# Kernel optimization log

Measured on AMD Instinct MI355X. Metric: run time of the kernel, lower is better.

The kernel has to match this reference:

```python
import jax, jax.numpy as jnp
import numpy as np

H_HEADS = 8
DIM_HEAD = 64


def setup_inputs() -> dict:
    key = jax.random.key(0)
    ks = jax.random.split(key, 5)
    b, c, Hs, Ws = 16, 32, 128, 128
    qd = H_HEADS * c              # 256 (heads*c = Linear in_features)
    inner = H_HEADS * DIM_HEAD    # 512
    s = 0.02                      # keep logits in a sane range
    return {
        "x": jax.random.normal(ks[0], (b, c, Hs, Ws), jnp.float32),
        "Wq": jax.random.normal(ks[1], (inner, qd), jnp.float32) * s,
        "Wkv": jax.random.normal(ks[2], (2 * inner, qd), jnp.float32) * s,
        "Wout": jax.random.normal(ks[3], (qd, inner), jnp.float32) * s,
        "bout": jax.random.normal(ks[4], (qd,), jnp.float32) * s,
    }


def _proj(arg, W, bias=None):
    # apply_operator_or_ffn for nn.Linear:
    # rearrange '(b h) n d -> b d (h n)', Linear over last dim, then 'b d n -> b n d'
    B, n, d = arg.shape
    bp = B // H_HEADS
    t = arg.reshape(bp, H_HEADS, n, d)
    t = jnp.transpose(t, (0, 3, 1, 2)).reshape(bp, d, H_HEADS * n)  # [b', d, h*n]
    y = t @ W.T
    if bias is not None:
        y = y + bias
    return jnp.transpose(y, (0, 2, 1))  # [b', out_features, d]


def _split_heads(t):
    # 'b (h d) n -> (b h) d n'
    bp, hd, n = t.shape
    return t.reshape(bp, H_HEADS, hd // H_HEADS, n).reshape(bp * H_HEADS, hd // H_HEADS, n)


def reference(x, Wq, Wkv, Wout, bout):
    b, c = x.shape[0], x.shape[1]
    spatial = x.shape[2:]
    N = int(np.prod(spatial))
    scale = DIM_HEAD ** -0.5
    xf = x.reshape(b, c, N)
    q = _proj(xf, Wq)              # [b/h, inner, N]
    kv = _proj(xf, Wkv)            # [b/h, 2*inner, N]
    inner = q.shape[1]
    k, v = kv[:, :inner], kv[:, inner:]
    qh, kh, vh = _split_heads(q), _split_heads(k), _split_heads(v)  # [b, DIM_HEAD, N]
    sim = jnp.einsum('bin,bjn->bij', qh, kh) * scale                 # [b, dh, dh]
    attn = jax.nn.softmax(sim, axis=-1)
    out = jnp.einsum('bnj,bjd->bnd', attn, vh)                       # [b, dh, N]
    out = _proj(out, Wout, bout)                                     # [b/h, h*c, N]
    return out.reshape(b, c, *spatial)
```

## Files before the change

### kernel.cpp

```cpp
#include <hip/hip_runtime.h>
#include <cstdint>
#include <cstddef>

using u16 = unsigned short;
using u32 = unsigned int;

typedef __attribute__((ext_vector_type(8))) short bf16x8;
typedef __attribute__((ext_vector_type(16))) float f32x16;

__device__ __forceinline__ u16 f2bf(float f) {
  union { float f; u32 i; } x; x.f = f;
  u32 r = (x.i + 0x7FFFu + ((x.i >> 16) & 1u)) >> 16;
  return (u16)r;
}
__device__ __forceinline__ bf16x8 ldbf16x8(const u16* p) {
  union { uint4 u; bf16x8 v; } t;
  t.u = *(const uint4*)p;
  return t.v;
}

constexpr int NP = 16384;


constexpr size_t OFF_C   = 0;
constexpr size_t OFF_T   = 131072;
constexpr size_t OFF_AT  = 393216;
constexpr size_t OFF_WE  = 458752;
constexpr size_t OFF_MT  = 720896;
constexpr size_t OFF_MA  = 851968;
constexpr size_t OFF_XB  = 917504;
constexpr size_t OFF_XBT = 5111808;
constexpr size_t OFF_CP1 = 9306112;
constexpr size_t NEED1   = (OFF_CP1 + 4194304) * 4;
constexpr size_t OFF_CP2 = 851968;
constexpr size_t NEED2   = (OFF_CP2 + 6291456) * 4;

__global__ __launch_bounds__(256)
void k0_cvt(const float* __restrict__ x, u16* __restrict__ XbF,
            u16* __restrict__ XbTF) {
  __shared__ u32 Fs[256 * 33];
  const int pc = blockIdx.x;
  const int g  = blockIdx.y;
  const int p0 = pc * 64;
  const float* __restrict__ Xg = x + (size_t)g * 256 * NP;
  u16* __restrict__ XbFg  = XbF  + (size_t)g * 256 * NP;
  u16* __restrict__ XbTFg = XbTF + (size_t)g * NP * 256;
  const int tid = threadIdx.x;
  const int f8i = tid & 7, rb = tid >> 3;
  const int sA = pc * 4 + (f8i >> 1);
  const int hA = f8i & 1;
  for (int pass = 0; pass < 8; ++pass) {
    const int row = rb + pass * 32;
    const size_t e0 = (size_t)row * NP + p0 + f8i * 8;
    float4 a = *(const float4*)(Xg + e0);
    float4 b = *(const float4*)(Xg + e0 + 4);
    const float v[8] = {a.x, a.y, a.z, a.w, b.x, b.y, b.z, b.w};
    uint4 s;
    s.x = (u32)f2bf(v[0]) | ((u32)f2bf(v[1]) << 16);
    s.y = (u32)f2bf(v[2]) | ((u32)f2bf(v[3]) << 16);
    s.z = (u32)f2bf(v[4]) | ((u32)f2bf(v[5]) << 16);
    s.w = (u32)f2bf(v[6]) | ((u32)f2bf(v[7]) << 16);
    const int panel = row >> 5, lc = row & 31;
    *(uint4*)(XbFg + (size_t)panel * 524288 + sA * 512 + hA * 256 + lc * 8) = s;
    u32* d = &Fs[row * 33 + f8i * 4];
    d[0] = s.x; d[1] = s.y; d[2] = s.z; d[3] = s.w;
  }
  __syncthreads();
  const int p = tid & 63, grp = tid >> 6;
  const int pp = p0 + p;
  const int panelT = pp >> 5, lcT = pp & 31;
  const u16* __restrict__ Fs16 = (const u16*)Fs;
  u16* dstT = XbTFg + (size_t)panelT * 8192 + lcT * 8;
  for (int c = 0; c < 4; ++c) {
    const int sT = grp * 4 + c;
    u32 w[8];
#pragma unroll
    for (int q = 0; q < 8; ++q) {
      const int f = grp * 64 + c * 16 + q * 2;
      u32 lo = Fs16[f * 66 + p];
      u32 hi = Fs16[(f + 1) * 66 + p];
      w[q] = lo | (hi << 16);
    }
    uint4 s0 = {w[0], w[1], w[2], w[3]};
    uint4 s1 = {w[4], w[5], w[6], w[7]};
    *(uint4*)(dstT + sT * 512)       = s0;
    *(uint4*)(dstT + sT * 512 + 256) = s1;
  }
}

__global__ __launch_bounds__(256)
void k1_mfma(const u16* __restrict__ XbF, float* __restrict__ Cpart) {
  const int tp = blockIdx.x;
  const int kc = blockIdx.y;
  const int g  = blockIdx.z;
  const int ti = tp >> 1, tj = tp & 1;
  const int tid = threadIdx.x;
  const int w = tid >> 6, half = (tid >> 5) & 1, lc = tid & 31;
  const int qi = w >> 1, qj = w & 1;
  const u16* __restrict__ Xg = XbF + (size_t)g * 256 * NP;
  const size_t koff = (size_t)kc * 16384 + half * 256 + lc * 8;
  const u16* A0 = Xg + (size_t)(ti * 4 + qi * 2 + 0) * 524288 + koff;
  const u16* A1 = Xg + (size_t)(ti * 4 + qi * 2 + 1) * 524288 + koff;
  const u16* B0 = Xg + (size_t)(tj * 4 + qj * 2 + 0) * 524288 + koff;
  const u16* B1 = Xg + (size_t)(tj * 4 + qj * 2 + 1) * 524288 + koff;
  f32x16 acc00, acc01, acc10, acc11;
#pragma unroll
  for (int i = 0; i < 16; ++i) {
    acc00[i] = 0.f; acc01[i] = 0.f; acc10[i] = 0.f; acc11[i] = 0.f;
  }
#pragma unroll 4
  for (int s = 0; s < 32; ++s) {
    bf16x8 a0 = ldbf16x8(A0 + s * 512);
    bf16x8 a1 = ldbf16x8(A1 + s * 512);
    bf16x8 b0 = ldbf16x8(B0 + s * 512);
    bf16x8 b1 = ldbf16x8(B1 + s * 512);
    acc00 = __builtin_amdgcn_mfma_f32_32x32x16_bf16(a0, b0, acc00, 0, 0, 0);
    acc01 = __builtin_amdgcn_mfma_f32_32x32x16_bf16(a0, b1, acc01, 0, 0, 0);
    acc10 = __builtin_amdgcn_mfma_f32_32x32x16_bf16(a1, b0, acc10, 0, 0, 0);
    acc11 = __builtin_amdgcn_mfma_f32_32x32x16_bf16(a1, b1, acc11, 0, 0, 0);
  }
  float* __restrict__ P = Cpart + (((size_t)g * 4 + tp) * 32 + kc) * 16384;
#pragma unroll
  for (int r = 0; r < 16; ++r) {
    const int rr = (r & 3) + 8 * (r >> 2) + 4 * half;
    const int row0 = qi * 64 + rr, col0 = qj * 64 + lc;
    P[(row0 +  0) * 128 + col0 +  0] = acc00[r];
    P[(row0 +  0) * 128 + col0 + 32] = acc01[r];
    P[(row0 + 32) * 128 + col0 +  0] = acc10[r];
    P[(row0 + 32) * 128 + col0 + 32] = acc11[r];
  }
}

__global__ __launch_bounds__(256)
void k1b_red(const float* __restrict__ Cpart, float* __restrict__ Cmat) {
  const int sl = blockIdx.x;
  const int tp = blockIdx.y;
  const int g  = blockIdx.z;
  const int ele = sl * 256 + threadIdx.x;
  const float* __restrict__ P =
      Cpart + (((size_t)g * 4 + tp) * 32) * 16384 + ele;
  float v = 0.f;
#pragma unroll
  for (int kc = 0; kc < 32; ++kc) v += P[(size_t)kc * 16384];
  const int ti = tp >> 1, tj = tp & 1;
  const int i = ele >> 7, j = ele & 127;
  Cmat[(size_t)g * 65536 + (size_t)(ti * 128 + i) * 256 + tj * 128 + j] = v;
}

__global__ __launch_bounds__(256)
void k1_gram(const float* __restrict__ x, float* __restrict__ Cpart) {
  __shared__ float As[32 * 132];
  __shared__ float Bs[32 * 132];
  const int kc = blockIdx.x, ty = blockIdx.y, g = blockIdx.z;
  const int i0 = (ty == 2) ? 128 : 0;
  const int j0 = (ty == 0) ? 0 : 128;
  const float* __restrict__ Xg = x + (size_t)g * 256 * NP;
  const int tid = threadIdx.x, lane = tid & 63, w = tid >> 6;
  const int wy = (w >> 1) * 64, wx = (w & 1) * 64;
  const int ly = (lane >> 3) * 8, lx = (lane & 7) * 8;
  float acc[8][8];
#pragma unroll
  for (int e = 0; e < 8; ++e)
#pragma unroll
    for (int f = 0; f < 8; ++f) acc[e][f] = 0.f;
  const int k8 = (tid & 3) * 8, rowb = tid >> 2, k0 = kc * 256;
  for (int s = 0; s < 8; ++s) {
    const int ks = k0 + s * 32;
#pragma unroll
    for (int pass = 0; pass < 2; ++pass) {
      const int row = rowb + pass * 64;
      const size_t ea = (size_t)(i0 + row) * NP + ks + k8;
      float4 a = *(const float4*)(Xg + ea);
      float4 b = *(const float4*)(Xg + ea + 4);
      As[(k8+0)*132+row]=a.x; As[(k8+1)*132+row]=a.y;
      As[(k8+2)*132+row]=a.z; As[(k8+3)*132+row]=a.w;
      As[(k8+4)*132+row]=b.x; As[(k8+5)*132+row]=b.y;
      As[(k8+6)*132+row]=b.z; As[(k8+7)*132+row]=b.w;
      const size_t eb = (size_t)(j0 + row) * NP + ks + k8;
      a = *(const float4*)(Xg + eb);
      b = *(const float4*)(Xg + eb + 4);
      Bs[(k8+0)*132+row]=a.x; Bs[(k8+1)*132+row]=a.y;
      Bs[(k8+2)*132+row]=a.z; Bs[(k8+3)*132+row]=a.w;
      Bs[(k8+4)*132+row]=b.x; Bs[(k8+5)*132+row]=b.y;
      Bs[(k8+6)*132+row]=b.z; Bs[(k8+7)*132+row]=b.w;
    }
    __syncthreads();
#pragma unroll 4
    for (int kk = 0; kk < 32; ++kk) {
      const float* ar = &As[kk * 132 + wy + ly];
      const float* br = &Bs[kk * 132 + wx + lx];
      float4 a0 = *(const float4*)(ar), a1 = *(const float4*)(ar + 4);
      float4 b0 = *(const float4*)(br), b1 = *(const float4*)(br + 4);
      const float av[8] = {a0.x,a0.y,a0.z,a0.w,a1.x,a1.y,a1.z,a1.w};
      const float bv[8] = {b0.x,b0.y,b0.z,b0.w,b1.x,b1.y,b1.z,b1.w};
#pragma unroll
      for (int e = 0; e < 8; ++e)
#pragma unroll
        for (int f = 0; f < 8; ++f) acc[e][f] += av[e] * bv[f];
    }
    __syncthreads();
  }
  float* __restrict__ P = Cpart + (((size_t)g * 3 + ty) * 64 + kc) * 16384;
#pragma unroll
  for (int e = 0; e < 8; ++e) {
    float* pr = P + (size_t)(wy + ly + e) * 128 + wx + lx;
    float4 s0 = {acc[e][0], acc[e][1], acc[e][2], acc[e][3]};
    float4 s1 = {acc[e][4], acc[e][5], acc[e][6], acc[e][7]};
    *(float4*)(pr)     = s0;
    *(float4*)(pr + 4) = s1;
  }
}

__global__ __launch_bounds__(256)
void k1b_reduce(const float* __restrict__ Cpart, float* __restrict__ Cmat) {
  const int sl = blockIdx.x, ty = blockIdx.y, g = blockIdx.z;
  const int ele = sl * 256 + threadIdx.x;
  const float* __restrict__ P =
      Cpart + (((size_t)g * 3 + ty) * 64) * 16384 + ele;
  float v = 0.f;
#pragma unroll 8
  for (int kc = 0; kc < 64; ++kc) v += P[(size_t)kc * 16384];
  const int i0 = (ty == 2) ? 128 : 0;
  const int j0 = (ty == 0) ? 0 : 128;
  const int i = ele >> 7, j = ele & 127;
  float* Cg = Cmat + (size_t)g * 65536;
  Cg[(size_t)(i0 + i) * 256 + (j0 + j)] = v;
  if (ty == 1) Cg[(size_t)(j0 + j) * 256 + (i0 + i)] = v;
}

__global__ __launch_bounds__(256)
void k1_gram_atomic(const float* __restrict__ x, float* __restrict__ Cmat) {
  __shared__ float As[32 * 132];
  __shared__ float Bs[32 * 132];
  const int kc = blockIdx.x, ty = blockIdx.y, g = blockIdx.z;
  const int i0 = (ty == 2) ? 128 : 0;
  const int j0 = (ty == 0) ? 0 : 128;
  const float* __restrict__ Xg = x + (size_t)g * 256 * NP;
  const int tid = threadIdx.x, lane = tid & 63, w = tid >> 6;
  const int wy = (w >> 1) * 64, wx = (w & 1) * 64;
  const int ly = (lane >> 3) * 8, lx = (lane & 7) * 8;
  float acc[8][8];
#pragma unroll
  for (int e = 0; e < 8; ++e)
#pragma unroll
    for (int f = 0; f < 8; ++f) acc[e][f] = 0.f;
  const int k8 = (tid & 3) * 8, rowb = tid >> 2, k0 = kc * 256;
  for (int s = 0; s < 8; ++s) {
    const int ks = k0 + s * 32;
#pragma unroll
    for (int pass = 0; pass < 2; ++pass) {
      const int row = rowb + pass * 64;
      const size_t ea = (size_t)(i0 + row) * NP + ks + k8;
      float4 a = *(const float4*)(Xg + ea);
      float4 b = *(const float4*)(Xg + ea + 4);
      As[(k8+0)*132+row]=a.x; As[(k8+1)*132+row]=a.y;
      As[(k8+2)*132+row]=a.z; As[(k8+3)*132+row]=a.w;
      As[(k8+4)*132+row]=b.x; As[(k8+5)*132+row]=b.y;
      As[(k8+6)*132+row]=b.z; As[(k8+7)*132+row]=b.w;
      const size_t eb = (size_t)(j0 + row) * NP + ks + k8;
      a = *(const float4*)(Xg + eb);
      b = *(const float4*)(Xg + eb + 4);
      Bs[(k8+0)*132+row]=a.x; Bs[(k8+1)*132+row]=a.y;
      Bs[(k8+2)*132+row]=a.z; Bs[(k8+3)*132+row]=a.w;
      Bs[(k8+4)*132+row]=b.x; Bs[(k8+5)*132+row]=b.y;
      Bs[(k8+6)*132+row]=b.z; Bs[(k8+7)*132+row]=b.w;
    }
    __syncthreads();
#pragma unroll 4
    for (int kk = 0; kk < 32; ++kk) {
      const float* ar = &As[kk * 132 + wy + ly];
      const float* br = &Bs[kk * 132 + wx + lx];
      float4 a0 = *(const float4*)(ar), a1 = *(const float4*)(ar + 4);
      float4 b0 = *(const float4*)(br), b1 = *(const float4*)(br + 4);
      const float av[8] = {a0.x,a0.y,a0.z,a0.w,a1.x,a1.y,a1.z,a1.w};
      const float bv[8] = {b0.x,b0.y,b0.z,b0.w,b1.x,b1.y,b1.z,b1.w};
#pragma unroll
      for (int e = 0; e < 8; ++e)
#pragma unroll
        for (int f = 0; f < 8; ++f) acc[e][f] += av[e] * bv[f];
    }
    __syncthreads();
  }
  float* Cg = Cmat + (size_t)g * 65536;
#pragma unroll
  for (int e = 0; e < 8; ++e)
#pragma unroll
    for (int f = 0; f < 8; ++f) {
      atomicAdd(&Cg[(i0+wy+ly+e)*256 + (j0+wx+lx+f)], acc[e][f]);
      if (ty == 1)
        atomicAdd(&Cg[(j0+wx+lx+f)*256 + (i0+wy+ly+e)], acc[e][f]);
    }
}

__global__ __launch_bounds__(256)
void kA_attn(const float* __restrict__ Wq, const float* __restrict__ Wkv,
             const float* __restrict__ Cmat, float* __restrict__ attn) {
  __shared__ float WqL[4 * 256];
  __shared__ float Ts[4 * 256];
  const int bh = blockIdx.x;
  const int ic = blockIdx.y;
  const int g = bh >> 3, hh = bh & 7;
  const int tid = threadIdx.x;
  const float* __restrict__ Cg = Cmat + (size_t)g * 65536;
  {
    const int r = tid >> 6, c4 = (tid & 63) * 4;
    *(float4*)(&WqL[r * 256 + c4]) =
        *(const float4*)(Wq + (size_t)(hh * 64 + ic * 4 + r) * 256 + c4);
  }
  __syncthreads();
  float acc[4] = {0.f, 0.f, 0.f, 0.f};
#pragma unroll 8
  for (int b = 0; b < 256; ++b) {
    const float cv = Cg[(size_t)b * 256 + tid];
#pragma unroll
    for (int r = 0; r < 4; ++r) acc[r] += WqL[r * 256 + b] * cv;
  }
#pragma unroll
  for (int r = 0; r < 4; ++r) Ts[r * 256 + tid] = acc[r];
  __syncthreads();
  const int r = tid >> 6, j = tid & 63;
  const float* __restrict__ Wk = Wkv + (size_t)(hh * 64 + j) * 256;
  float s = 0.f;
#pragma unroll 4
  for (int a4 = 0; a4 < 64; ++a4) {
    float4 w = *(const float4*)(Wk + a4 * 4);
    const float* t4 = &Ts[r * 256 + a4 * 4];
    s += t4[0] * w.x + t4[1] * w.y + t4[2] * w.z + t4[3] * w.w;
  }
  s *= 0.125f;
  float m = s;
#pragma unroll
  for (int off = 32; off; off >>= 1) m = fmaxf(m, __shfl_xor(m, off));
  const float e = __expf(s - m);
  float sum = e;
#pragma unroll
  for (int off = 32; off; off >>= 1) sum += __shfl_xor(sum, off);
  attn[((size_t)bh * 64 + ic * 4 + r) * 64 + j] = e / sum;
}

__global__ __launch_bounds__(256)
void kB_m(const float* __restrict__ Wout, const float* __restrict__ Wkv,
          const float* __restrict__ attn, float* __restrict__ Mp) {
  __shared__ float AtL[64 * 64];
  __shared__ float WoL[16 * 64];
  __shared__ float UL[16 * 64];
  const int bh = blockIdx.x;
  const int cc = blockIdx.y;
  const int g = bh >> 3, hh = bh & 7;
  const int tid = threadIdx.x;
  {
    const float* __restrict__ A = attn + (size_t)bh * 4096;
#pragma unroll
    for (int q = 0; q < 4; ++q)
      *(float4*)(&AtL[q * 1024 + tid * 4]) =
          *(const float4*)(A + q * 1024 + tid * 4);
  }
  {
    const int co_l = tid >> 4, i4 = (tid & 15) * 4;
    *(float4*)(&WoL[co_l * 64 + i4]) =
        *(const float4*)(Wout + (size_t)(cc * 16 + co_l) * 512 + hh * 64 + i4);
  }
  __syncthreads();
  const int j = tid & 63, cw = tid >> 6;
  float u4[4] = {0.f, 0.f, 0.f, 0.f};
#pragma unroll 4
  for (int i = 0; i < 64; ++i) {
    const float av = AtL[i * 64 + j];
#pragma unroll
    for (int u = 0; u < 4; ++u) u4[u] += WoL[(cw * 4 + u) * 64 + i] * av;
  }
  __syncthreads();
#pragma unroll
  for (int u = 0; u < 4; ++u) UL[(cw * 4 + u) * 64 + j] = u4[u];
  __syncthreads();
  float acc[16];
#pragma unroll
  for (int c = 0; c < 16; ++c) acc[c] = 0.f;
#pragma unroll 4
  for (int j2 = 0; j2 < 64; ++j2) {
    const float wv = Wkv[(size_t)(512 + hh * 64 + j2) * 256 + tid];
#pragma unroll
    for (int c = 0; c < 16; ++c) acc[c] += UL[c * 64 + j2] * wv;
  }
  float* __restrict__ P =
      Mp + (((size_t)g * 8 + hh) * 256 + cc * 16) * 256 + tid;
#pragma unroll
  for (int c = 0; c < 16; ++c) P[(size_t)c * 256] = acc[c];
}

__global__ __launch_bounds__(256)
void kC_red(const float* __restrict__ Mp, u16* __restrict__ MA) {
  const int panel = blockIdx.x >> 2;
  const int q     = blockIdx.x & 3;
  const int g     = blockIdx.y;
  const int tid = threadIdx.x;
  const float* __restrict__ Pg = Mp + (size_t)g * 8 * 65536;
  u16* __restrict__ Mg = MA + (size_t)g * 65536;
  const int item = tid + q * 256;
  const int lc = item & 31;
  const int co = panel * 32 + lc;
  const int b0 = (item >> 5) * 8;
  float v[8] = {0.f, 0.f, 0.f, 0.f, 0.f, 0.f, 0.f, 0.f};
#pragma unroll
  for (int hd = 0; hd < 8; ++hd) {
    const float* p = Pg + (size_t)hd * 65536 + (size_t)co * 256 + b0;
    float4 a = *(const float4*)(p);
    float4 b = *(const float4*)(p + 4);
    v[0] += a.x; v[1] += a.y; v[2] += a.z; v[3] += a.w;
    v[4] += b.x; v[5] += b.y; v[6] += b.z; v[7] += b.w;
  }
  uint4 sdat;
  sdat.x = (u32)f2bf(v[0]) | ((u32)f2bf(v[1]) << 16);
  sdat.y = (u32)f2bf(v[2]) | ((u32)f2bf(v[3]) << 16);
  sdat.z = (u32)f2bf(v[4]) | ((u32)f2bf(v[5]) << 16);
  sdat.w = (u32)f2bf(v[6]) | ((u32)f2bf(v[7]) << 16);
  *(uint4*)(Mg + (size_t)panel * 8192 + (size_t)item * 8) = sdat;
}

__global__ __launch_bounds__(256) void k2_T(const float* __restrict__ Wq,
                                            const float* __restrict__ Cmat,
                                            float* __restrict__ T) {
  const int bh = blockIdx.x;
  const int ic = blockIdx.y;
  const int g = bh >> 3, hh = bh & 7;
  const int tid = threadIdx.x;
  const float* __restrict__ Cg = Cmat + (size_t)g * 65536;
  const int r0 = hh * 64 + ic * 4;
  float acc[4] = {0.f, 0.f, 0.f, 0.f};
#pragma unroll 8
  for (int b = 0; b < 256; ++b) {
    const float cv = Cg[(size_t)b * 256 + tid];
#pragma unroll
    for (int ii = 0; ii < 4; ++ii)
      acc[ii] += Wq[(size_t)(r0 + ii) * 256 + b] * cv;
  }
#pragma unroll
  for (int ii = 0; ii < 4; ++ii)
    T[((size_t)bh * 64 + ic * 4 + ii) * 256 + tid] = acc[ii];
}

__global__ __launch_bounds__(256) void k3_sim(const float* __restrict__ Wkv,
                                              const float* __restrict__ T,
                                              float* __restrict__ simattn) {
  __shared__ float Ts[64 * 256];
  const int bh = blockIdx.x;
  const int jc = blockIdx.y;
  const int hh = bh & 7;
  const int tid = threadIdx.x;
  {
    const int f4i = tid & 63;
    const int rwb = tid >> 6;
    for (int pass = 0; pass < 16; ++pass) {
      const int row = rwb + pass * 4;
      float4 v = *(const float4*)(T + ((size_t)bh * 64 + row) * 256 + f4i * 4);
      const int a0 = f4i * 4;
      const float vv[4] = {v.x, v.y, v.z, v.w};
#pragma unroll
      for (int e = 0; e < 4; ++e) {
        const int a = a0 + e;
        Ts[row * 256 + (a & ~31) + ((a + row) & 31)] = vv[e];
      }
    }
  }
  __syncthreads();
  const int i  = tid & 63;
  const int jq = tid >> 6;
  const int jb = jc * 16 + jq * 4;
  float acc[4] = {0.f, 0.f, 0.f, 0.f};
#pragma unroll 4
  for (int a = 0; a < 256; ++a) {
    const float tv = Ts[i * 256 + (a & ~31) + ((a + i) & 31)];
#pragma unroll
    for (int jj = 0; jj < 4; ++jj)
      acc[jj] += Wkv[(size_t)(hh * 64 + jb + jj) * 256 + a] * tv;
  }
#pragma unroll
  for (int jj = 0; jj < 4; ++jj)
    simattn[((size_t)bh * 64 + i) * 64 + jb + jj] = acc[jj] * 0.125f;
}

__global__ __launch_bounds__(64) void k3b_softmax(float* __restrict__ simattn) {
  const int bh = blockIdx.x;
  const int i  = threadIdx.x;
  float* row = simattn + ((size_t)bh * 64 + i) * 64;
  float v[64];
  float m = -1e30f;
#pragma unroll
  for (int j = 0; j < 64; ++j) { v[j] = row[j]; m = fmaxf(m, v[j]); }
  float s = 0.f;
#pragma unroll
  for (int j = 0; j < 64; ++j) { v[j] = __expf(v[j] - m); s += v[j]; }
  const float inv = 1.0f / s;
#pragma unroll
  for (int j = 0; j < 64; ++j) row[j] = v[j] * inv;
}

__global__ __launch_bounds__(256) void k4_we(const float* __restrict__ Wout,
                                             const float* __restrict__ attn,
                                             float* __restrict__ WeT) {
  __shared__ float WL[256 * 64];
  const int jc = blockIdx.x;
  const int hh = blockIdx.y;
  const int g  = blockIdx.z;
  const int bh = g * 8 + hh;
  const int tid = threadIdx.x;
  {
    const int f4i = tid & 15;
    const int cb  = tid >> 4;
    for (int pass = 0; pass < 16; ++pass) {
      const int co = cb + pass * 16;
      float4 v = *(const float4*)(Wout + (size_t)co * 512 + hh * 64 + f4i * 4);
      const int a0 = f4i * 4;
      const float vv[4] = {v.x, v.y, v.z, v.w};
#pragma unroll
      for (int e = 0; e < 4; ++e)
        WL[co * 64 + ((a0 + e + co) & 63)] = vv[e];
    }
  }
  __syncthreads();
  const int jb = jc * 8;
  float acc[8] = {0.f, 0.f, 0.f, 0.f, 0.f, 0.f, 0.f, 0.f};
#pragma unroll 4
  for (int i = 0; i < 64; ++i) {
    const float wv = WL[tid * 64 + ((i + tid) & 63)];
#pragma unroll
    for (int je = 0; je < 8; ++je)
      acc[je] += attn[((size_t)bh * 64 + i) * 64 + jb + je] * wv;
  }
#pragma unroll
  for (int je = 0; je < 8; ++je)
    WeT[(size_t)g * 131072 + (size_t)(hh * 64 + jb + je) * 256 + tid] =
        acc[je];
}

__global__ __launch_bounds__(256)
void k5a_part(const float* __restrict__ Wkv, const float* __restrict__ WeT,
              float* __restrict__ Mp) {
  const int bc = blockIdx.x;
  const int oc = blockIdx.y;
  const int g  = blockIdx.z;
  const int tid = threadIdx.x;
  const int b0 = bc * 4;
  const float* __restrict__ Weg = WeT + (size_t)g * 131072;
  float acc[4] = {0.f, 0.f, 0.f, 0.f};
#pragma unroll 8
  for (int u = 0; u < 32; ++u) {
    const int o = oc * 32 + u;
    const float wv = Weg[(size_t)o * 256 + tid];
    const float* __restrict__ vr = Wkv + (size_t)(512 + o) * 256 + b0;
    acc[0] += vr[0] * wv;
    acc[1] += vr[1] * wv;
    acc[2] += vr[2] * wv;
    acc[3] += vr[3] * wv;
  }
#pragma unroll
  for (int be = 0; be < 4; ++be)
    Mp[(((size_t)g * 16 + oc) * 256 + b0 + be) * 256 + tid] = acc[be];
}

__global__ __launch_bounds__(256)
void k5b_red(const float* __restrict__ Mp, float* __restrict__ Mt,
             u16* __restrict__ MA) {
  const int b = blockIdx.x;
  const int g = blockIdx.y;
  const int tid = threadIdx.x;
  const float* __restrict__ P =
      Mp + ((size_t)g * 16 * 256 + b) * 256 + tid;
  float v = 0.f;
#pragma unroll
  for (int oc = 0; oc < 16; ++oc) v += P[(size_t)oc * 65536];
  Mt[(size_t)g * 65536 + (size_t)b * 256 + tid] = v;
  MA[(size_t)g * 65536 + (size_t)tid * 256 + b] = f2bf(v);
}

__global__ __launch_bounds__(256) void k5_serial(const float* __restrict__ Wkv,
                                                 const float* __restrict__ WeT,
                                                 float* __restrict__ Mt,
                                                 u16* __restrict__ MA) {
  const int bc = blockIdx.x;
  const int g  = blockIdx.y;
  const int tid = threadIdx.x;
  const int b0 = bc * 4;
  const float* __restrict__ Weg = WeT + (size_t)g * 131072;
  float acc[4] = {0.f, 0.f, 0.f, 0.f};
#pragma unroll 4
  for (int o = 0; o < 512; ++o) {
    const float wv = Weg[(size_t)o * 256 + tid];
    const float* __restrict__ vr = Wkv + (size_t)(512 + o) * 256 + b0;
    acc[0] += vr[0] * wv;
    acc[1] += vr[1] * wv;
    acc[2] += vr[2] * wv;
    acc[3] += vr[3] * wv;
  }
#pragma unroll
  for (int be = 0; be < 4; ++be) {
    Mt[(size_t)g * 65536 + (size_t)(b0 + be) * 256 + tid] = acc[be];
    MA[(size_t)g * 65536 + (size_t)tid * 256 + b0 + be] = f2bf(acc[be]);
  }
}

__global__ __launch_bounds__(256)
void k6_mfma(const u16* __restrict__ XbTF, const u16* __restrict__ MA,
             const float* __restrict__ bout, float* __restrict__ out) {
  const int pb = blockIdx.x;
  const int cb = blockIdx.y;
  const int g  = blockIdx.z;
  const int tid = threadIdx.x;
  const int w = tid >> 6, half = (tid >> 5) & 1, lc = tid & 31;
  const int p0  = pb * 128 + w * 32;
  const int co0 = cb * 128;
  const u16* __restrict__ Ap = XbTF + (size_t)g * NP * 256 +
                               (size_t)(pb * 4 + w) * 8192 + half * 256 +
                               lc * 8;
  const u16* __restrict__ Bp = MA + (size_t)g * 65536 +
                               (size_t)cb * 32768 + half * 256 + lc * 8;
  f32x16 acc[4];
#pragma unroll
  for (int t = 0; t < 4; ++t)
#pragma unroll
    for (int i = 0; i < 16; ++i) acc[t][i] = 0.f;
#pragma unroll 2
  for (int s = 0; s < 16; ++s) {
    bf16x8 a = ldbf16x8(Ap + s * 512);
#pragma unroll
    for (int t = 0; t < 4; ++t) {
      bf16x8 b = ldbf16x8(Bp + (size_t)t * 8192 + s * 512);
      acc[t] = __builtin_amdgcn_mfma_f32_32x32x16_bf16(a, b, acc[t], 0, 0, 0);
    }
  }
#pragma unroll
  for (int t = 0; t < 4; ++t) {
    const int co = co0 + t * 32 + lc;
    const float bo = bout[co];
    float* __restrict__ ocol =
        out + ((size_t)(g * 256 + co)) * NP + p0 + 4 * half;
#pragma unroll
    for (int rg = 0; rg < 4; ++rg) {
      float4 v = {acc[t][rg * 4 + 0] + bo, acc[t][rg * 4 + 1] + bo,
                  acc[t][rg * 4 + 2] + bo, acc[t][rg * 4 + 3] + bo};
      *(float4*)(ocol + rg * 8) = v;
    }
  }
}

__global__ __launch_bounds__(256)
void k6_apply(const float* __restrict__ x, const float* __restrict__ Mt,
              const float* __restrict__ bout, float* __restrict__ out) {
  __shared__ float As[32 * 132];
  __shared__ float Bs[32 * 132];
  const int pc = blockIdx.x;
  const int oy = blockIdx.y;
  const int g  = blockIdx.z;
  const int p0 = pc * 128;
  const int o0 = oy * 128;
  const float* __restrict__ Xg = x + (size_t)g * 256 * NP;
  const float* __restrict__ Mg = Mt + (size_t)g * 65536;
  const int tid  = threadIdx.x;
  const int lane = tid & 63;
  const int w    = tid >> 6;
  const int wy = (w >> 1) * 64;
  const int wx = (w & 1) * 64;
  const int ly = (lane >> 3) * 8;
  const int lx = (lane & 7) * 8;
  float acc[8][8];
#pragma unroll
  for (int e = 0; e < 8; ++e)
#pragma unroll
    for (int f = 0; f < 8; ++f) acc[e][f] = 0.f;
  const int c4 = (tid & 31) * 4;
  const int kb = tid >> 5;
  for (int s = 0; s < 8; ++s) {
#pragma unroll
    for (int r = 0; r < 4; ++r) {
      const int kk = kb + r * 8;
      const int f  = s * 32 + kk;
      *(float4*)&As[kk * 132 + c4] =
          *(const float4*)(Mg + (size_t)f * 256 + o0 + c4);
      *(float4*)&Bs[kk * 132 + c4] =
          *(const float4*)(Xg + (size_t)f * NP + p0 + c4);
    }
    __syncthreads();
#pragma unroll 4
    for (int kk = 0; kk < 32; ++kk) {
      const float* __restrict__ ar = &As[kk * 132 + wy + ly];
      const float* __restrict__ br = &Bs[kk * 132 + wx + lx];
      float4 a0 = *(const float4*)(ar);
      float4 a1 = *(const float4*)(ar + 4);
      float4 b0 = *(const float4*)(br);
      float4 b1 = *(const float4*)(br + 4);
      const float av[8] = {a0.x, a0.y, a0.z, a0.w, a1.x, a1.y, a1.z, a1.w};
      const float bv[8] = {b0.x, b0.y, b0.z, b0.w, b1.x, b1.y, b1.z, b1.w};
#pragma unroll
      for (int e = 0; e < 8; ++e)
#pragma unroll
        for (int f = 0; f < 8; ++f) acc[e][f] += av[e] * bv[f];
    }
    __syncthreads();
  }
#pragma unroll
  for (int e = 0; e < 8; ++e) {
    const int co = o0 + wy + ly + e;
    const float bo = bout[co];
    float* __restrict__ orow =
        out + ((size_t)(g * 256 + co)) * NP + p0 + wx + lx;
    float4 s0 = {acc[e][0] + bo, acc[e][1] + bo, acc[e][2] + bo,
                 acc[e][3] + bo};
    float4 s1 = {acc[e][4] + bo, acc[e][5] + bo, acc[e][6] + bo,
                 acc[e][7] + bo};
    *(float4*)(orow)     = s0;
    *(float4*)(orow + 4) = s1;
  }
}

extern "C" void kernel_launch(void* const* d_in, const int* in_sizes, int n_in,
                              void* d_out, int out_size, void* d_ws,
                              size_t ws_size, hipStream_t stream) {
  const float* x    = (const float*)d_in[0];
  const float* Wq   = (const float*)d_in[1];
  const float* Wkv  = (const float*)d_in[2];
  const float* Wout = (const float*)d_in[3];
  const float* bout = (const float*)d_in[4];
  float* out = (float*)d_out;
  float* ws  = (float*)d_ws;

  float* C    = ws + OFF_C;
  float* T    = ws + OFF_T;
  float* att  = ws + OFF_AT;
  float* WeT  = ws + OFF_WE;
  float* Mt   = ws + OFF_MT;
  u16*   MA   = (u16*)(ws + OFF_MA);
  u16*   Xb   = (u16*)(ws + OFF_XB);
  u16*   XbT  = (u16*)(ws + OFF_XBT);
  float* Cp1  = ws + OFF_CP1;
  float* Cp2  = ws + OFF_CP2;

  const bool mfma_path = (ws_size >= NEED1);
  const bool splitk    = (ws_size >= NEED2);

  if (mfma_path) {
    k0_cvt<<<dim3(256, 2), 256, 0, stream>>>(x, Xb, XbT);
    k1_mfma<<<dim3(4, 32, 2), 256, 0, stream>>>(Xb, Cp1);
    k1b_red<<<dim3(64, 4, 2), 256, 0, stream>>>(Cp1, C);
    kA_attn<<<dim3(16, 16), 256, 0, stream>>>(Wq, Wkv, C, att);
    kB_m<<<dim3(16, 16), 256, 0, stream>>>(Wout, Wkv, att, Cp1);
    kC_red<<<dim3(32, 2), 256, 0, stream>>>(Cp1, MA);
    k6_mfma<<<dim3(128, 2, 2), 256, 0, stream>>>(XbT, MA, bout, out);
    return;
  }

  if (splitk) {
    k1_gram<<<dim3(64, 3, 2), 256, 0, stream>>>(x, Cp2);
    k1b_reduce<<<dim3(64, 3, 2), 256, 0, stream>>>(Cp2, C);
  } else {
    hipMemsetAsync(C, 0, 131072 * sizeof(float), stream);
    k1_gram_atomic<<<dim3(64, 3, 2), 256, 0, stream>>>(x, C);
  }
  k2_T<<<dim3(16, 16), 256, 0, stream>>>(Wq, C, T);
  k3_sim<<<dim3(16, 4), 256, 0, stream>>>(Wkv, T, att);
  k3b_softmax<<<dim3(16), 64, 0, stream>>>(att);
  k4_we<<<dim3(8, 8, 2), 256, 0, stream>>>(Wout, att, WeT);
  if (splitk) {
    k5a_part<<<dim3(64, 16, 2), 256, 0, stream>>>(Wkv, WeT, Cp2);
    k5b_red<<<dim3(256, 2), 256, 0, stream>>>(Cp2, Mt, MA);
  } else {
    k5_serial<<<dim3(64, 2), 256, 0, stream>>>(Wkv, WeT, Mt, MA);
  }
  k6_apply<<<dim3(128, 2, 2), 256, 0, stream>>>(x, Mt, bout, out);
}
```

Baseline: 159.3 us.

## Fuse all pipeline stages into one cooperative persistent kernel with grid syncs

Merges the seven separate kernels (bf16 convert, Gram MFMA, split-K reduce, attention, M build, M reduce, output MFMA) into a single cooperative kernel of 512 blocks, with grid.sync() between stages. This removes per-kernel launch overhead and inter-kernel gaps in a pipeline made of many small stages. In exchange, many stages use only 64–256 of the 512 blocks and each grid barrier has its own cost. The NEED1 workspace threshold is bumped slightly, and the old multi-kernel path stays as a fallback if the cooperative launch fails.

Measured after the change: 491.6 us. +208.7%, slower.

```diff
diff --git a/kernel.cpp b/kernel.cpp
--- a/kernel.cpp
+++ b/kernel.cpp
@@ -1,6 +1,9 @@
 #include <hip/hip_runtime.h>
+#include <hip/hip_cooperative_groups.h>
 #include <cstdint>
 #include <cstddef>
+
+namespace cg = cooperative_groups;
 
 using u16 = unsigned short;
 using u32 = unsigned int;
@@ -31,9 +34,283 @@
 constexpr size_t OFF_XB  = 917504;
 constexpr size_t OFF_XBT = 5111808;
 constexpr size_t OFF_CP1 = 9306112;
-constexpr size_t NEED1   = (OFF_CP1 + 4194304) * 4;
+constexpr size_t NEED1   = (OFF_CP1 + 4194304 + 4) * 4;
 constexpr size_t OFF_CP2 = 851968;
 constexpr size_t NEED2   = (OFF_CP2 + 6291456) * 4;
+
+__global__ __launch_bounds__(256, 2)
+void fused_all(const float* __restrict__ x, const float* __restrict__ Wq,
+               const float* __restrict__ Wkv, const float* __restrict__ Wout,
+               const float* __restrict__ bout, float* __restrict__ out,
+               u16* __restrict__ XbF, u16* __restrict__ XbTF,
+               float* __restrict__ Cmat, float* __restrict__ attn,
+               u16* __restrict__ MA, float* __restrict__ Cpart) {
+  __shared__ __align__(16) u32 shm[256 * 33];
+  cg::grid_group grid = cg::this_grid();
+  const int bid = blockIdx.x;
+  const int tid = threadIdx.x;
+
+  {
+    const int pc = bid >> 1, g = bid & 1;
+    const int p0 = pc * 64;
+    const float* __restrict__ Xg = x + (size_t)g * 256 * NP;
+    u16* __restrict__ XbFg  = XbF  + (size_t)g * 256 * NP;
+    u16* __restrict__ XbTFg = XbTF + (size_t)g * NP * 256;
+    const int f8i = tid & 7, rb = tid >> 3;
+    const int sA = pc * 4 + (f8i >> 1);
+    const int hA = f8i & 1;
+    u32* Fs = shm;
+    for (int pass = 0; pass < 8; ++pass) {
+      const int row = rb + pass * 32;
+      const size_t e0 = (size_t)row * NP + p0 + f8i * 8;
+      float4 a = *(const float4*)(Xg + e0);
+      float4 b = *(const float4*)(Xg + e0 + 4);
+      const float v[8] = {a.x, a.y, a.z, a.w, b.x, b.y, b.z, b.w};
+      uint4 s;
+      s.x = (u32)f2bf(v[0]) | ((u32)f2bf(v[1]) << 16);
+      s.y = (u32)f2bf(v[2]) | ((u32)f2bf(v[3]) << 16);
+      s.z = (u32)f2bf(v[4]) | ((u32)f2bf(v[5]) << 16);
+      s.w = (u32)f2bf(v[6]) | ((u32)f2bf(v[7]) << 16);
+      const int panel = row >> 5, lc = row & 31;
+      *(uint4*)(XbFg + (size_t)panel * 524288 + sA * 512 + hA * 256 + lc * 8) =
+          s;
+      u32* d = &Fs[row * 33 + f8i * 4];
+      d[0] = s.x; d[1] = s.y; d[2] = s.z; d[3] = s.w;
+    }
+    __syncthreads();
+    const int p = tid & 63, grp = tid >> 6;
+    const int pp = p0 + p;
+    const int panelT = pp >> 5, lcT = pp & 31;
+    const u16* __restrict__ Fs16 = (const u16*)Fs;
+    u16* dstT = XbTFg + (size_t)panelT * 8192 + lcT * 8;
+    for (int c = 0; c < 4; ++c) {
+      const int sT = grp * 4 + c;
+      u32 w[8];
+#pragma unroll
+      for (int q = 0; q < 8; ++q) {
+        const int f = grp * 64 + c * 16 + q * 2;
+        u32 lo = Fs16[f * 66 + p];
+        u32 hi = Fs16[(f + 1) * 66 + p];
+        w[q] = lo | (hi << 16);
+      }
+      uint4 s0 = {w[0], w[1], w[2], w[3]};
+      uint4 s1 = {w[4], w[5], w[6], w[7]};
+      *(uint4*)(dstT + sT * 512)       = s0;
+      *(uint4*)(dstT + sT * 512 + 256) = s1;
+    }
+  }
+  grid.sync();
+
+  if (bid < 256) {
+    const int tp = bid >> 6, kc = (bid >> 1) & 31, g = bid & 1;
+    const int ti = tp >> 1, tj = tp & 1;
+    const int w = tid >> 6, half = (tid >> 5) & 1, lc = tid & 31;
+    const int qi = w >> 1, qj = w & 1;
+    const u16* __restrict__ Xg = XbF + (size_t)g * 256 * NP;
+    const size_t koff = (size_t)kc * 16384 + half * 256 + lc * 8;
+    const u16* A0 = Xg + (size_t)(ti * 4 + qi * 2 + 0) * 524288 + koff;
+    const u16* A1 = Xg + (size_t)(ti * 4 + qi * 2 + 1) * 524288 + koff;
+    const u16* B0 = Xg + (size_t)(tj * 4 + qj * 2 + 0) * 524288 + koff;
+    const u16* B1 = Xg + (size_t)(tj * 4 + qj * 2 + 1) * 524288 + koff;
+    f32x16 acc00, acc01, acc10, acc11;
+#pragma unroll
+    for (int i = 0; i < 16; ++i) {
+      acc00[i] = 0.f; acc01[i] = 0.f; acc10[i] = 0.f; acc11[i] = 0.f;
+    }
+#pragma unroll 4
+    for (int s = 0; s < 32; ++s) {
+      bf16x8 a0 = ldbf16x8(A0 + s * 512);
+      bf16x8 a1 = ldbf16x8(A1 + s * 512);
+      bf16x8 b0 = ldbf16x8(B0 + s * 512);
+      bf16x8 b1 = ldbf16x8(B1 + s * 512);
+      acc00 = __builtin_amdgcn_mfma_f32_32x32x16_bf16(a0, b0, acc00, 0, 0, 0);
+      acc01 = __builtin_amdgcn_mfma_f32_32x32x16_bf16(a0, b1, acc01, 0, 0, 0);
+      acc10 = __builtin_amdgcn_mfma_f32_32x32x16_bf16(a1, b0, acc10, 0, 0, 0);
+      acc11 = __builtin_amdgcn_mfma_f32_32x32x16_bf16(a1, b1, acc11, 0, 0, 0);
+    }
+    float* __restrict__ P = Cpart + (((size_t)g * 4 + tp) * 32 + kc) * 16384;
+#pragma unroll
+    for (int r = 0; r < 16; ++r) {
+      const int rr = (r & 3) + 8 * (r >> 2) + 4 * half;
+      const int row0 = qi * 64 + rr, col0 = qj * 64 + lc;
+      P[(row0 +  0) * 128 + col0 +  0] = acc00[r];
+      P[(row0 +  0) * 128 + col0 + 32] = acc01[r];
+      P[(row0 + 32) * 128 + col0 +  0] = acc10[r];
+      P[(row0 + 32) * 128 + col0 + 32] = acc11[r];
+    }
+  }
+  grid.sync();
+
+  {
+    const int sl = bid >> 3, tp = (bid >> 1) & 3, g = bid & 1;
+    const int ele = sl * 256 + tid;
+    const float* __restrict__ P =
+        Cpart + (((size_t)g * 4 + tp) * 32) * 16384 + ele;
+    float v = 0.f;
+#pragma unroll
+    for (int kc = 0; kc < 32; ++kc) v += P[(size_t)kc * 16384];
+    const int ti = tp >> 1, tj = tp & 1;
+    const int i = ele >> 7, j = ele & 127;
+    Cmat[(size_t)g * 65536 + (size_t)(ti * 128 + i) * 256 + tj * 128 + j] = v;
+  }
+  grid.sync();
+
+  if (bid < 256) {
+    float* WqL = (float*)shm;
+    float* Ts  = (float*)shm + 1024;
+    const int bh = bid >> 4, ic = bid & 15;
+    const int g = bh >> 3, hh = bh & 7;
+    const float* __restrict__ Cg = Cmat + (size_t)g * 65536;
+    {
+      const int r = tid >> 6, c4 = (tid & 63) * 4;
+      *(float4*)(&WqL[r * 256 + c4]) =
+          *(const float4*)(Wq + (size_t)(hh * 64 + ic * 4 + r) * 256 + c4);
+    }
+    __syncthreads();
+    float acc[4] = {0.f, 0.f, 0.f, 0.f};
+#pragma unroll 8
+    for (int b = 0; b < 256; ++b) {
+      const float cv = Cg[(size_t)b * 256 + tid];
+#pragma unroll
+      for (int r = 0; r < 4; ++r) acc[r] += WqL[r * 256 + b] * cv;
+    }
+#pragma unroll
+    for (int r = 0; r < 4; ++r) Ts[r * 256 + tid] = acc[r];
+    __syncthreads();
+    const int r = tid >> 6, j = tid & 63;
+    const float* __restrict__ Wk = Wkv + (size_t)(hh * 64 + j) * 256;
+    float s = 0.f;
+#pragma unroll 4
+    for (int a4 = 0; a4 < 64; ++a4) {
+      float4 w = *(const float4*)(Wk + a4 * 4);
+      const float* t4 = &Ts[r * 256 + a4 * 4];
+      s += t4[0] * w.x + t4[1] * w.y + t4[2] * w.z + t4[3] * w.w;
+    }
+    s *= 0.125f;
+    float m = s;
+#pragma unroll
+    for (int off = 32; off; off >>= 1) m = fmaxf(m, __shfl_xor(m, off));
+    const float e = __expf(s - m);
+    float sum = e;
+#pragma unroll
+    for (int off = 32; off; off >>= 1) sum += __shfl_xor(sum, off);
+    attn[((size_t)bh * 64 + ic * 4 + r) * 64 + j] = e / sum;
+  }
+  grid.sync();
+
+  if (bid < 256) {
+    float* AtL = (float*)shm;
+    float* WoL = (float*)shm + 4096;
+    float* UL  = (float*)shm + 5120;
+    const int bh = bid >> 4, cc = bid & 15;
+    const int g = bh >> 3, hh = bh & 7;
+    {
+      const float* __restrict__ A = attn + (size_t)bh * 4096;
+#pragma unroll
+      for (int q = 0; q < 4; ++q)
+        *(float4*)(&AtL[q * 1024 + tid * 4]) =
+            *(const float4*)(A + q * 1024 + tid * 4);
+    }
+    {
+      const int co_l = tid >> 4, i4 = (tid & 15) * 4;
+      *(float4*)(&WoL[co_l * 64 + i4]) = *(const float4*)(
+          Wout + (size_t)(cc * 16 + co_l) * 512 + hh * 64 + i4);
+    }
+    __syncthreads();
+    const int j = tid & 63, cw = tid >> 6;
+    float u4[4] = {0.f, 0.f, 0.f, 0.f};
+#pragma unroll 4
+    for (int i = 0; i < 64; ++i) {
+      const float av = AtL[i * 64 + j];
+#pragma unroll
+      for (int u = 0; u < 4; ++u) u4[u] += WoL[(cw * 4 + u) * 64 + i] * av;
+    }
+    __syncthreads();
+#pragma unroll
+    for (int u = 0; u < 4; ++u) UL[(cw * 4 + u) * 64 + j] = u4[u];
+    __syncthreads();
+    float acc[16];
+#pragma unroll
+    for (int c = 0; c < 16; ++c) acc[c] = 0.f;
+#pragma unroll 4
+    for (int j2 = 0; j2 < 64; ++j2) {
+      const float wv = Wkv[(size_t)(512 + hh * 64 + j2) * 256 + tid];
+#pragma unroll
+      for (int c = 0; c < 16; ++c) acc[c] += UL[c * 64 + j2] * wv;
+    }
+    float* __restrict__ P =
+        Cpart + (((size_t)g * 8 + hh) * 256 + cc * 16) * 256 + tid;
+#pragma unroll
+    for (int c = 0; c < 16; ++c) P[(size_t)c * 256] = acc[c];
+  }
+  grid.sync();
+
+  if (bid < 64) {
+    const int xx = bid >> 1, g = bid & 1;
+    const int panel = xx >> 2, q = xx & 3;
+    const float* __restrict__ Pg = Cpart + (size_t)g * 8 * 65536;
+    u16* __restrict__ Mg = MA + (size_t)g * 65536;
+    const int item = tid + q * 256;
+    const int lc = item & 31;
+    const int co = panel * 32 + lc;
+    const int b0 = (item >> 5) * 8;
+    float v[8] = {0.f, 0.f, 0.f, 0.f, 0.f, 0.f, 0.f, 0.f};
+#pragma unroll
+    for (int hd = 0; hd < 8; ++hd) {
+      const float* p = Pg + (size_t)hd * 65536 + (size_t)co * 256 + b0;
+      float4 a = *(const float4*)(p);
+      float4 b = *(const float4*)(p + 4);
+      v[0] += a.x; v[1] += a.y; v[2] += a.z; v[3] += a.w;
+      v[4] += b.x; v[5] += b.y; v[6] += b.z; v[7] += b.w;
+    }
+    uint4 sdat;
+    sdat.x = (u32)f2bf(v[0]) | ((u32)f2bf(v[1]) << 16);
+    sdat.y = (u32)f2bf(v[2]) | ((u32)f2bf(v[3]) << 16);
+    sdat.z = (u32)f2bf(v[4]) | ((u32)f2bf(v[5]) << 16);
+    sdat.w = (u32)f2bf(v[6]) | ((u32)f2bf(v[7]) << 16);
+    *(uint4*)(Mg + (size_t)panel * 8192 + (size_t)item * 8) = sdat;
+  }
+  grid.sync();
+
+  {
+    const int pb = bid >> 2, cb = (bid >> 1) & 1, g = bid & 1;
+    const int w = tid >> 6, half = (tid >> 5) & 1, lc = tid & 31;
+    const int p0  = pb * 128 + w * 32;
+    const int co0 = cb * 128;
+    const u16* __restrict__ Ap = XbTF + (size_t)g * NP * 256 +
+                                 (size_t)(pb * 4 + w) * 8192 + half * 256 +
+                                 lc * 8;
+    const u16* __restrict__ Bp =
+        MA + (size_t)g * 65536 + (size_t)cb * 32768 + half * 256 + lc * 8;
+    f32x16 acc[4];
+#pragma unroll
+    for (int t = 0; t < 4; ++t)
+#pragma unroll
+      for (int i = 0; i < 16; ++i) acc[t][i] = 0.f;
+#pragma unroll 2
+    for (int s = 0; s < 16; ++s) {
+      bf16x8 a = ldbf16x8(Ap + s * 512);
+#pragma unroll
+      for (int t = 0; t < 4; ++t) {
+        bf16x8 b = ldbf16x8(Bp + (size_t)t * 8192 + s * 512);
+        acc[t] = __builtin_amdgcn_mfma_f32_32x32x16_bf16(a, b, acc[t], 0, 0, 0);
+      }
+    }
+#pragma unroll
+    for (int t = 0; t < 4; ++t) {
+      const int co = co0 + t * 32 + lc;
+      const float bo = bout[co];
+      float* __restrict__ ocol =
+          out + ((size_t)(g * 256 + co)) * NP + p0 + 4 * half;
+#pragma unroll
+      for (int rg = 0; rg < 4; ++rg) {
+        float4 v = {acc[t][rg * 4 + 0] + bo, acc[t][rg * 4 + 1] + bo,
+                    acc[t][rg * 4 + 2] + bo, acc[t][rg * 4 + 3] + bo};
+        *(float4*)(ocol + rg * 8) = v;
+      }
+    }
+  }
+}
 
 __global__ __launch_bounds__(256)
 void k0_cvt(const float* __restrict__ x, u16* __restrict__ XbF,
@@ -148,6 +425,175 @@
 }
 
 __global__ __launch_bounds__(256)
+void kA_attn(const float* __restrict__ Wq, const float* __restrict__ Wkv,
+             const float* __restrict__ Cmat, float* __restrict__ attn) {
+  __shared__ float WqL[4 * 256];
+  __shared__ float Ts[4 * 256];
+  const int bh = blockIdx.x;
+  const int ic = blockIdx.y;
+  const int g = bh >> 3, hh = bh & 7;
+  const int tid = threadIdx.x;
+  const float* __restrict__ Cg = Cmat + (size_t)g * 65536;
+  {
+    const int r = tid >> 6, c4 = (tid & 63) * 4;
+    *(float4*)(&WqL[r * 256 + c4]) =
+        *(const float4*)(Wq + (size_t)(hh * 64 + ic * 4 + r) * 256 + c4);
+  }
+  __syncthreads();
+  float acc[4] = {0.f, 0.f, 0.f, 0.f};
+#pragma unroll 8
+  for (int b = 0; b < 256; ++b) {
+    const float cv = Cg[(size_t)b * 256 + tid];
+#pragma unroll
+    for (int r = 0; r < 4; ++r) acc[r] += WqL[r * 256 + b] * cv;
+  }
+#pragma unroll
+  for (int r = 0; r < 4; ++r) Ts[r * 256 + tid] = acc[r];
+  __syncthreads();
+  const int r = tid >> 6, j = tid & 63;
+  const float* __restrict__ Wk = Wkv + (size_t)(hh * 64 + j) * 256;
+  float s = 0.f;
+#pragma unroll 4
+  for (int a4 = 0; a4 < 64; ++a4) {
+    float4 w = *(const float4*)(Wk + a4 * 4);
+    const float* t4 = &Ts[r * 256 + a4 * 4];
+    s += t4[0] * w.x + t4[1] * w.y + t4[2] * w.z + t4[3] * w.w;
+  }
+  s *= 0.125f;
+  float m = s;
+#pragma unroll
+  for (int off = 32; off; off >>= 1) m = fmaxf(m, __shfl_xor(m, off));
+  const float e = __expf(s - m);
+  float sum = e;
+#pragma unroll
+  for (int off = 32; off; off >>= 1) sum += __shfl_xor(sum, off);
+  attn[((size_t)bh * 64 + ic * 4 + r) * 64 + j] = e / sum;
+}
+
+__global__ __launch_bounds__(256)
+void kB_m(const float* __restrict__ Wout, const float* __restrict__ Wkv,
+          const float* __restrict__ attn, float* __restrict__ Mp) {
+  __shared__ float AtL[64 * 64];
+  __shared__ float WoL[16 * 64];
+  __shared__ float UL[16 * 64];
+  const int bh = blockIdx.x;
+  const int cc = blockIdx.y;
+  const int g = bh >> 3, hh = bh & 7;
+  const int tid = threadIdx.x;
+  {
+    const float* __restrict__ A = attn + (size_t)bh * 4096;
+#pragma unroll
+    for (int q = 0; q < 4; ++q)
+      *(float4*)(&AtL[q * 1024 + tid * 4]) =
+          *(const float4*)(A + q * 1024 + tid * 4);
+  }
+  {
+    const int co_l = tid >> 4, i4 = (tid & 15) * 4;
+    *(float4*)(&WoL[co_l * 64 + i4]) =
+        *(const float4*)(Wout + (size_t)(cc * 16 + co_l) * 512 + hh * 64 + i4);
+  }
+  __syncthreads();
+  const int j = tid & 63, cw = tid >> 6;
+  float u4[4] = {0.f, 0.f, 0.f, 0.f};
+#pragma unroll 4
+  for (int i = 0; i < 64; ++i) {
+    const float av = AtL[i * 64 + j];
+#pragma unroll
+    for (int u = 0; u < 4; ++u) u4[u] += WoL[(cw * 4 + u) * 64 + i] * av;
+  }
+  __syncthreads();
+#pragma unroll
+  for (int u = 0; u < 4; ++u) UL[(cw * 4 + u) * 64 + j] = u4[u];
+  __syncthreads();
+  float acc[16];
+#pragma unroll
+  for (int c = 0; c < 16; ++c) acc[c] = 0.f;
+#pragma unroll 4
+  for (int j2 = 0; j2 < 64; ++j2) {
+    const float wv = Wkv[(size_t)(512 + hh * 64 + j2) * 256 + tid];
+#pragma unroll
+    for (int c = 0; c < 16; ++c) acc[c] += UL[c * 64 + j2] * wv;
+  }
+  float* __restrict__ P =
+      Mp + (((size_t)g * 8 + hh) * 256 + cc * 16) * 256 + tid;
+#pragma unroll
+  for (int c = 0; c < 16; ++c) P[(size_t)c * 256] = acc[c];
+}
+
+__global__ __launch_bounds__(256)
+void kC_red(const float* __restrict__ Mp, u16* __restrict__ MA) {
+  const int panel = blockIdx.x >> 2;
+  const int q     = blockIdx.x & 3;
+  const int g     = blockIdx.y;
+  const int tid = threadIdx.x;
+  const float* __restrict__ Pg = Mp + (size_t)g * 8 * 65536;
+  u16* __restrict__ Mg = MA + (size_t)g * 65536;
+  const int item = tid + q * 256;
+  const int lc = item & 31;
+  const int co = panel * 32 + lc;
+  const int b0 = (item >> 5) * 8;
+  float v[8] = {0.f, 0.f, 0.f, 0.f, 0.f, 0.f, 0.f, 0.f};
+#pragma unroll
+  for (int hd = 0; hd < 8; ++hd) {
+    const float* p = Pg + (size_t)hd * 65536 + (size_t)co * 256 + b0;
+    float4 a = *(const float4*)(p);
+    float4 b = *(const float4*)(p + 4);
+    v[0] += a.x; v[1] += a.y; v[2] += a.z; v[3] += a.w;
+    v[4] += b.x; v[5] += b.y; v[6] += b.z; v[7] += b.w;
+  }
+  uint4 sdat;
+  sdat.x = (u32)f2bf(v[0]) | ((u32)f2bf(v[1]) << 16);
+  sdat.y = (u32)f2bf(v[2]) | ((u32)f2bf(v[3]) << 16);
+  sdat.z = (u32)f2bf(v[4]) | ((u32)f2bf(v[5]) << 16);
+  sdat.w = (u32)f2bf(v[6]) | ((u32)f2bf(v[7]) << 16);
+  *(uint4*)(Mg + (size_t)panel * 8192 + (size_t)item * 8) = sdat;
+}
+
+__global__ __launch_bounds__(256)
+void k6_mfma(const u16* __restrict__ XbTF, const u16* __restrict__ MA,
+             const float* __restrict__ bout, float* __restrict__ out) {
+  const int pb = blockIdx.x;
+  const int cb = blockIdx.y;
+  const int g  = blockIdx.z;
+  const int tid = threadIdx.x;
+  const int w = tid >> 6, half = (tid >> 5) & 1, lc = tid & 31;
+  const int p0  = pb * 128 + w * 32;
+  const int co0 = cb * 128;
+  const u16* __restrict__ Ap = XbTF + (size_t)g * NP * 256 +
+                               (size_t)(pb * 4 + w) * 8192 + half * 256 +
+                               lc * 8;
+  const u16* __restrict__ Bp = MA + (size_t)g * 65536 +
+                               (size_t)cb * 32768 + half * 256 + lc * 8;
+  f32x16 acc[4];
+#pragma unroll
+  for (int t = 0; t < 4; ++t)
+#pragma unroll
+    for (int i = 0; i < 16; ++i) acc[t][i] = 0.f;
+#pragma unroll 2
+  for (int s = 0; s < 16; ++s) {
+    bf16x8 a = ldbf16x8(Ap + s * 512);
+#pragma unroll
+    for (int t = 0; t < 4; ++t) {
+      bf16x8 b = ldbf16x8(Bp + (size_t)t * 8192 + s * 512);
+      acc[t] = __builtin_amdgcn_mfma_f32_32x32x16_bf16(a, b, acc[t], 0, 0, 0);
+    }
+  }
+#pragma unroll
+  for (int t = 0; t < 4; ++t) {
+    const int co = co0 + t * 32 + lc;
+    const float bo = bout[co];
+    float* __restrict__ ocol =
+        out + ((size_t)(g * 256 + co)) * NP + p0 + 4 * half;
+#pragma unroll
+    for (int rg = 0; rg < 4; ++rg) {
+      float4 v = {acc[t][rg * 4 + 0] + bo, acc[t][rg * 4 + 1] + bo,
+                  acc[t][rg * 4 + 2] + bo, acc[t][rg * 4 + 3] + bo};
+      *(float4*)(ocol + rg * 8) = v;
+    }
+  }
+}
+
+__global__ __launch_bounds__(256)
 void k1_gram(const float* __restrict__ x, float* __restrict__ Cpart) {
   __shared__ float As[32 * 132];
   __shared__ float Bs[32 * 132];
@@ -292,131 +738,6 @@
     }
 }
 
-__global__ __launch_bounds__(256)
-void kA_attn(const float* __restrict__ Wq, const float* __restrict__ Wkv,
-             const float* __restrict__ Cmat, float* __restrict__ attn) {
-  __shared__ float WqL[4 * 256];
-  __shared__ float Ts[4 * 256];
-  const int bh = blockIdx.x;
-  const int ic = blockIdx.y;
-  const int g = bh >> 3, hh = bh & 7;
-  const int tid = threadIdx.x;
-  const float* __restrict__ Cg = Cmat + (size_t)g * 65536;
-  {
-    const int r = tid >> 6, c4 = (tid & 63) * 4;
-    *(float4*)(&WqL[r * 256 + c4]) =
-        *(const float4*)(Wq + (size_t)(hh * 64 + ic * 4 + r) * 256 + c4);
-  }
-  __syncthreads();
-  float acc[4] = {0.f, 0.f, 0.f, 0.f};
-#pragma unroll 8
-  for (int b = 0; b < 256; ++b) {
-    const float cv = Cg[(size_t)b * 256 + tid];
-#pragma unroll
-    for (int r = 0; r < 4; ++r) acc[r] += WqL[r * 256 + b] * cv;
-  }
-#pragma unroll
-  for (int r = 0; r < 4; ++r) Ts[r * 256 + tid] = acc[r];
-  __syncthreads();
-  const int r = tid >> 6, j = tid & 63;
-  const float* __restrict__ Wk = Wkv + (size_t)(hh * 64 + j) * 256;
-  float s = 0.f;
-#pragma unroll 4
-  for (int a4 = 0; a4 < 64; ++a4) {
-    float4 w = *(const float4*)(Wk + a4 * 4);
-    const float* t4 = &Ts[r * 256 + a4 * 4];
-    s += t4[0] * w.x + t4[1] * w.y + t4[2] * w.z + t4[3] * w.w;
-  }
-  s *= 0.125f;
-  float m = s;
-#pragma unroll
-  for (int off = 32; off; off >>= 1) m = fmaxf(m, __shfl_xor(m, off));
-  const float e = __expf(s - m);
-  float sum = e;
-#pragma unroll
-  for (int off = 32; off; off >>= 1) sum += __shfl_xor(sum, off);
-  attn[((size_t)bh * 64 + ic * 4 + r) * 64 + j] = e / sum;
-}
-
-__global__ __launch_bounds__(256)
-void kB_m(const float* __restrict__ Wout, const float* __restrict__ Wkv,
-          const float* __restrict__ attn, float* __restrict__ Mp) {
-  __shared__ float AtL[64 * 64];
-  __shared__ float WoL[16 * 64];
-  __shared__ float UL[16 * 64];
-  const int bh = blockIdx.x;
-  const int cc = blockIdx.y;
-  const int g = bh >> 3, hh = bh & 7;
-  const int tid = threadIdx.x;
-  {
-    const float* __restrict__ A = attn + (size_t)bh * 4096;
-#pragma unroll
-    for (int q = 0; q < 4; ++q)
-      *(float4*)(&AtL[q * 1024 + tid * 4]) =
-          *(const float4*)(A + q * 1024 + tid * 4);
-  }
-  {
-    const int co_l = tid >> 4, i4 = (tid & 15) * 4;
-    *(float4*)(&WoL[co_l * 64 + i4]) =
-        *(const float4*)(Wout + (size_t)(cc * 16 + co_l) * 512 + hh * 64 + i4);
-  }
-  __syncthreads();
-  const int j = tid & 63, cw = tid >> 6;
-  float u4[4] = {0.f, 0.f, 0.f, 0.f};
-#pragma unroll 4
-  for (int i = 0; i < 64; ++i) {
-    const float av = AtL[i * 64 + j];
-#pragma unroll
-    for (int u = 0; u < 4; ++u) u4[u] += WoL[(cw * 4 + u) * 64 + i] * av;
-  }
-  __syncthreads();
-#pragma unroll
-  for (int u = 0; u < 4; ++u) UL[(cw * 4 + u) * 64 + j] = u4[u];
-  __syncthreads();
-  float acc[16];
-#pragma unroll
-  for (int c = 0; c < 16; ++c) acc[c] = 0.f;
-#pragma unroll 4
-  for (int j2 = 0; j2 < 64; ++j2) {
-    const float wv = Wkv[(size_t)(512 + hh * 64 + j2) * 256 + tid];
-#pragma unroll
-    for (int c = 0; c < 16; ++c) acc[c] += UL[c * 64 + j2] * wv;
-  }
-  float* __restrict__ P =
-      Mp + (((size_t)g * 8 + hh) * 256 + cc * 16) * 256 + tid;
-#pragma unroll
-  for (int c = 0; c < 16; ++c) P[(size_t)c * 256] = acc[c];
-}
-
-__global__ __launch_bounds__(256)
-void kC_red(const float* __restrict__ Mp, u16* __restrict__ MA) {
-  const int panel = blockIdx.x >> 2;
-  const int q     = blockIdx.x & 3;
-  const int g     = blockIdx.y;
-  const int tid = threadIdx.x;
-  const float* __restrict__ Pg = Mp + (size_t)g * 8 * 65536;
-  u16* __restrict__ Mg = MA + (size_t)g * 65536;
-  const int item = tid + q * 256;
-  const int lc = item & 31;
-  const int co = panel * 32 + lc;
-  const int b0 = (item >> 5) * 8;
-  float v[8] = {0.f, 0.f, 0.f, 0.f, 0.f, 0.f, 0.f, 0.f};
-#pragma unroll
-  for (int hd = 0; hd < 8; ++hd) {
-    const float* p = Pg + (size_t)hd * 65536 + (size_t)co * 256 + b0;
-    float4 a = *(const float4*)(p);
-    float4 b = *(const float4*)(p + 4);
-    v[0] += a.x; v[1] += a.y; v[2] += a.z; v[3] += a.w;
-    v[4] += b.x; v[5] += b.y; v[6] += b.z; v[7] += b.w;
-  }
-  uint4 sdat;
-  sdat.x = (u32)f2bf(v[0]) | ((u32)f2bf(v[1]) << 16);
-  sdat.y = (u32)f2bf(v[2]) | ((u32)f2bf(v[3]) << 16);
-  sdat.z = (u32)f2bf(v[4]) | ((u32)f2bf(v[5]) << 16);
-  sdat.w = (u32)f2bf(v[6]) | ((u32)f2bf(v[7]) << 16);
-  *(uint4*)(Mg + (size_t)panel * 8192 + (size_t)item * 8) = sdat;
-}
-
 __global__ __launch_bounds__(256) void k2_T(const float* __restrict__ Wq,
                                             const float* __restrict__ Cmat,
                                             float* __restrict__ T) {
@@ -596,50 +917,6 @@
   for (int be = 0; be < 4; ++be) {
     Mt[(size_t)g * 65536 + (size_t)(b0 + be) * 256 + tid] = acc[be];
     MA[(size_t)g * 65536 + (size_t)tid * 256 + b0 + be] = f2bf(acc[be]);
-  }
-}
-
-__global__ __launch_bounds__(256)
-void k6_mfma(const u16* __restrict__ XbTF, const u16* __restrict__ MA,
-             const float* __restrict__ bout, float* __restrict__ out) {
-  const int pb = blockIdx.x;
-  const int cb = blockIdx.y;
-  const int g  = blockIdx.z;
-  const int tid = threadIdx.x;
-  const int w = tid >> 6, half = (tid >> 5) & 1, lc = tid & 31;
-  const int p0  = pb * 128 + w * 32;
-  const int co0 = cb * 128;
-  const u16* __restrict__ Ap = XbTF + (size_t)g * NP * 256 +
-                               (size_t)(pb * 4 + w) * 8192 + half * 256 +
-                               lc * 8;
-  const u16* __restrict__ Bp = MA + (size_t)g * 65536 +
-                               (size_t)cb * 32768 + half * 256 + lc * 8;
-  f32x16 acc[4];
-#pragma unroll
-  for (int t = 0; t < 4; ++t)
-#pragma unroll
-    for (int i = 0; i < 16; ++i) acc[t][i] = 0.f;
-#pragma unroll 2
-  for (int s = 0; s < 16; ++s) {
-    bf16x8 a = ldbf16x8(Ap + s * 512);
-#pragma unroll
-    for (int t = 0; t < 4; ++t) {
-      bf16x8 b = ldbf16x8(Bp + (size_t)t * 8192 + s * 512);
-      acc[t] = __builtin_amdgcn_mfma_f32_32x32x16_bf16(a, b, acc[t], 0, 0, 0);
-    }
-  }
-#pragma unroll
-  for (int t = 0; t < 4; ++t) {
-    const int co = co0 + t * 32 + lc;
-    const float bo = bout[co];
-    float* __restrict__ ocol =
-        out + ((size_t)(g * 256 + co)) * NP + p0 + 4 * half;
-#pragma unroll
-    for (int rg = 0; rg < 4; ++rg) {
-      float4 v = {acc[t][rg * 4 + 0] + bo, acc[t][rg * 4 + 1] + bo,
-                  acc[t][rg * 4 + 2] + bo, acc[t][rg * 4 + 3] + bo};
-      *(float4*)(ocol + rg * 8) = v;
-    }
   }
 }
 
@@ -738,6 +1015,13 @@
   const bool splitk    = (ws_size >= NEED2);
 
   if (mfma_path) {
+    void* args[] = {(void*)&x,   (void*)&Wq,  (void*)&Wkv, (void*)&Wout,
+                    (void*)&bout,(void*)&out, (void*)&Xb,  (void*)&XbT,
+                    (void*)&C,   (void*)&att, (void*)&MA,  (void*)&Cp1};
+    hipError_t err = hipLaunchCooperativeKernel(
+        (const void*)fused_all, dim3(512), dim3(256), args, 0, stream);
+    if (err == hipSuccess) return;
+    (void)hipGetLastError();
     k0_cvt<<<dim3(256, 2), 256, 0, stream>>>(x, Xb, XbT);
     k1_mfma<<<dim3(4, 32, 2), 256, 0, stream>>>(Xb, Cp1);
     k1b_red<<<dim3(64, 4, 2), 256, 0, stream>>>(Cp1, C);
```
